# Kernel tuning notes

Hardware: AMD Instinct MI355X
Metric: run time of the kernel (lower is better)

The kernel has to match this reference:

```python
import jax, jax.numpy as jnp
import numpy as np

I_DECAY = 0.95
STAG_THRESH = 0.95
MAX_GATE = 0.6
MIN_I_GATE = 0.25
EPS = 1e-12


def setup_inputs() -> dict:
    key = jax.random.key(0)
    ks = jax.random.split(key, 9)
    B, T, D_IN, D_OUT = 4, 2048, 2048, 2048
    x = jax.random.normal(ks[0], (B, T, D_IN), dtype=jnp.float32)
    s = 1.0 / np.sqrt(D_IN)
    Wp = jax.random.uniform(ks[1], (D_IN, D_OUT), jnp.float32, -s, s)
    Wi = jax.random.uniform(ks[2], (D_IN, D_OUT), jnp.float32, -s, s) * 0.3
    Wd = jax.random.uniform(ks[3], (D_IN, D_OUT), jnp.float32, -s, s) * 0.3
    gate_w = jax.random.uniform(ks[4], (D_IN, 3), jnp.float32, -s, s)
    gate_b = jnp.array([0.5, 0.0, 0.0], dtype=jnp.float32)
    kick_vec = jax.random.normal(ks[5], (D_OUT,), dtype=jnp.float32) * 0.01
    kick_w = jax.random.uniform(ks[6], (D_IN, 1), jnp.float32, -s, s)
    kick_b = jnp.full((1,), -2.0, dtype=jnp.float32)
    bias = jnp.zeros((D_OUT,), dtype=jnp.float32)
    return {"x": x, "Wp": Wp, "Wi": Wi, "Wd": Wd, "gate_w": gate_w,
            "gate_b": gate_b, "kick_vec": kick_vec, "kick_w": kick_w,
            "kick_b": kick_b, "bias": bias}


def _ema_integral(x, decay):
    # x: [B,T,D] -> time-major scan; integral[0] = x[0]
    xt = jnp.swapaxes(x, 0, 1)  # [T,B,D]

    def step(carry, xcur):
        new = decay * carry + (1.0 - decay) * xcur
        return new, new

    init = xt[0]
    _, rest = jax.lax.scan(step, init, xt[1:])
    integral = jnp.concatenate([init[None], rest], axis=0)
    return jnp.swapaxes(integral, 0, 1)  # [B,T,D]


def reference(x, Wp, Wi, Wd, gate_w, gate_b, kick_vec, kick_w, kick_b, bias):
    B, T, D = x.shape
    # --- EMA integral (linear recurrence over T) ---
    integral = _ema_integral(x, I_DECAY)

    # --- stagnation-aware derivative ---
    diff = jnp.concatenate(
        [jnp.zeros_like(x[:, :1]), x[:, 1:] - x[:, :-1]], axis=1)
    x_norm = x / jnp.maximum(
        jnp.linalg.norm(x, axis=-1, keepdims=True), EPS)
    cos_sim = jnp.concatenate(
        [jnp.zeros((B, 1), x.dtype),
         jnp.sum(x_norm[:, 1:] * x_norm[:, :-1], axis=-1)], axis=1)  # [B,T]
    stagnation = (cos_sim > STAG_THRESH).astype(x.dtype)
    kick_strength = jax.nn.sigmoid(
        jnp.einsum('btd,do->bto', x, kick_w) + kick_b)[..., 0]  # [B,T]
    derivative = diff + (stagnation * kick_strength)[..., None] * kick_vec

    # --- gates: softmax -> clamp max -> clamp I min -> renormalize ---
    g = jax.nn.softmax(jnp.einsum('btd,dg->btg', x, gate_w) + gate_b, axis=-1)
    g = jnp.minimum(g, MAX_GATE)
    g = g.at[..., 1].set(jnp.maximum(g[..., 1], MIN_I_GATE))
    g = g / jnp.sum(g, axis=-1, keepdims=True)

    out = (g[..., 0:1] * jnp.einsum('btd,do->bto', x, Wp)
           + g[..., 1:2] * jnp.einsum('btd,do->bto', integral, Wi)
           + g[..., 2:3] * jnp.einsum('btd,do->bto', derivative, Wd))
    return out + bias
```

## Files before the change

kernel.cpp:

```cpp
#include <hip/hip_runtime.h>

#define DH 2048
#define TT 2048
#define BB 4
#define MROWS 8192
#define KTOT 6144
#define NCH 128
#define LCH 16
#define POW95_L 0.44012667f

typedef __attribute__((ext_vector_type(8))) short bf16x8;
typedef __attribute__((ext_vector_type(4))) float f32x4;

__device__ __forceinline__ unsigned short f2bf(float f) {
  union { float f; unsigned int u; } v; v.f = f;
  unsigned int u = v.u;
  return (unsigned short)((u + 0x7FFFu + ((u >> 16) & 1u)) >> 16);
}

__device__ __forceinline__ void gld16(const unsigned short* g, unsigned short* l) {
  __builtin_amdgcn_global_load_lds((const __attribute__((address_space(1))) void*)g,
                                   (__attribute__((address_space(3))) void*)l, 16, 0, 0);
}

__global__ __launch_bounds__(256) void prep_w(const float* __restrict__ Wp,
                                              const float* __restrict__ Wi,
                                              const float* __restrict__ Wd,
                                              const float* __restrict__ kick_vec,
                                              unsigned short* __restrict__ Wt,
                                              float* __restrict__ kvWd) {
  __shared__ float tile[64][65];
  int bid = blockIdx.x;
  int mat = bid >> 10;
  int t2 = bid & 1023;
  int dt = (t2 >> 5) * 64;
  int ot = (t2 & 31) * 64;
  const float* W = (mat == 0) ? Wp : ((mat == 1) ? Wi : Wd);
  int kbase = mat * DH;
  int tid = threadIdx.x;
  int r = tid >> 4;
  int c4 = (tid & 15) * 4;
#pragma unroll
  for (int i = 0; i < 4; ++i) {
    int rr = r + i * 16;
    float4 v = *(const float4*)&W[(size_t)(dt + rr) * DH + ot + c4];
    tile[rr][c4 + 0] = v.x; tile[rr][c4 + 1] = v.y;
    tile[rr][c4 + 2] = v.z; tile[rr][c4 + 3] = v.w;
  }
  __syncthreads();
  int o = tid >> 3;
  int d8 = (tid & 7) * 8;
#pragma unroll
  for (int pass = 0; pass < 2; ++pass) {
    int oo = o + pass * 32;
    union { unsigned short u[8]; uint4 v; } pk;
#pragma unroll
    for (int i = 0; i < 8; ++i) pk.u[i] = f2bf(tile[d8 + i][oo]);
    *(uint4*)&Wt[(size_t)(ot + oo) * KTOT + kbase + dt + d8] = pk.v;
  }
  if (mat == 2 && tid < 64) {
    float s = 0.f;
#pragma unroll 8
    for (int dd = 0; dd < 64; ++dd) s += kick_vec[dt + dd] * tile[dd][tid];
    atomicAdd(&kvWd[ot + tid], s);
  }
}

__global__ __launch_bounds__(256) void rowstats_kernel(const float* __restrict__ x,
                                                       const float* __restrict__ gate_w,
                                                       const float* __restrict__ gate_b,
                                                       const float* __restrict__ kick_w,
                                                       const float* __restrict__ kick_b,
                                                       float* __restrict__ rs) {
  int r = blockIdx.x;
  int t = r & (TT - 1);
  const float* xr = x + (size_t)r * DH;
  const float* xq = xr - DH;
  const bool hp = (t != 0);
  int tid = threadIdx.x;
  float a0 = 0, a1 = 0, a2 = 0, ak = 0, axx = 0, apx = 0, app = 0;
#pragma unroll
  for (int it = 0; it < 2; ++it) {
    int d0 = (tid + it * 256) * 4;
    float4 xv = *(const float4*)(xr + d0);
    float4 pv = hp ? *(const float4*)(xq + d0) : make_float4(0.f, 0.f, 0.f, 0.f);
    float4 q0 = *(const float4*)(gate_w + (size_t)d0 * 3);
    float4 q1 = *(const float4*)(gate_w + (size_t)d0 * 3 + 4);
    float4 q2 = *(const float4*)(gate_w + (size_t)d0 * 3 + 8);
    float4 kw = *(const float4*)(kick_w + d0);
    float xa[4] = {xv.x, xv.y, xv.z, xv.w};
    float pa[4] = {pv.x, pv.y, pv.z, pv.w};
    a0 += xa[0] * q0.x + xa[1] * q0.w + xa[2] * q1.z + xa[3] * q2.y;
    a1 += xa[0] * q0.y + xa[1] * q1.x + xa[2] * q1.w + xa[3] * q2.z;
    a2 += xa[0] * q0.z + xa[1] * q1.y + xa[2] * q2.x + xa[3] * q2.w;
    ak += xa[0] * kw.x + xa[1] * kw.y + xa[2] * kw.z + xa[3] * kw.w;
#pragma unroll
    for (int j = 0; j < 4; ++j) {
      axx += xa[j] * xa[j];
      apx += xa[j] * pa[j];
      app += pa[j] * pa[j];
    }
  }
#pragma unroll
  for (int off = 32; off > 0; off >>= 1) {
    a0 += __shfl_xor(a0, off); a1 += __shfl_xor(a1, off);
    a2 += __shfl_xor(a2, off); ak += __shfl_xor(ak, off);
    axx += __shfl_xor(axx, off); apx += __shfl_xor(apx, off);
    app += __shfl_xor(app, off);
  }
  __shared__ float red[4][7];
  int wv = tid >> 6;
  if ((tid & 63) == 0) {
    red[wv][0] = a0; red[wv][1] = a1; red[wv][2] = a2; red[wv][3] = ak;
    red[wv][4] = axx; red[wv][5] = apx; red[wv][6] = app;
  }
  __syncthreads();
  if (tid == 0) {
    float v[7];
#pragma unroll
    for (int i = 0; i < 7; ++i) v[i] = red[0][i] + red[1][i] + red[2][i] + red[3][i];
    float l0 = v[0] + gate_b[0], l1 = v[1] + gate_b[1], l2 = v[2] + gate_b[2];
    float mx = fmaxf(l0, fmaxf(l1, l2));
    float e0 = expf(l0 - mx), e1 = expf(l1 - mx), e2 = expf(l2 - mx);
    float inv = 1.f / (e0 + e1 + e2);
    float G0 = fminf(e0 * inv, 0.6f);
    float G1 = fminf(e1 * inv, 0.6f);
    float G2 = fminf(e2 * inv, 0.6f);
    G1 = fmaxf(G1, 0.25f);
    float inv2 = 1.f / (G0 + G1 + G2);
    G0 *= inv2; G1 *= inv2; G2 *= inv2;
    float ks = 1.f / (1.f + expf(-(v[3] + kick_b[0])));
    float nn = fmaxf(sqrtf(v[4]), 1e-12f) * fmaxf(sqrtf(v[6]), 1e-12f);
    float cs = hp ? (v[5] / nn) : 0.f;
    float cc = (cs > 0.95f) ? (G2 * ks) : 0.f;
    *(float4*)(rs + (size_t)r * 4) = make_float4(G0, G1, G2, cc);
  }
}

__global__ __launch_bounds__(256) void ema_carry(const float* __restrict__ x,
                                                 float* __restrict__ cp) {
  int gid = blockIdx.x * 256 + threadIdx.x;
  int d = (gid & 511) * 4;
  int ch = (gid >> 9) & (NCH - 1);
  int b = gid >> 16;
  const float* xp = x + ((size_t)b * TT + (size_t)ch * LCH) * DH + d;
  float J0, J1, J2, J3;
  int tstart;
  if (ch == 0) {
    float4 v = *(const float4*)xp;
    J0 = v.x; J1 = v.y; J2 = v.z; J3 = v.w;
    tstart = 1;
  } else {
    J0 = J1 = J2 = J3 = 0.f;
    tstart = 0;
  }
#pragma unroll 4
  for (int t = tstart; t < LCH; ++t) {
    float4 v = *(const float4*)(xp + (size_t)t * DH);
    J0 = 0.95f * J0 + 0.05f * v.x;
    J1 = 0.95f * J1 + 0.05f * v.y;
    J2 = 0.95f * J2 + 0.05f * v.z;
    J3 = 0.95f * J3 + 0.05f * v.w;
  }
  *(float4*)&cp[((size_t)b * NCH + ch) * DH + d] = make_float4(J0, J1, J2, J3);
}

__global__ __launch_bounds__(256) void ema_prefix(float* __restrict__ cp) {
  int gid = blockIdx.x * 256 + threadIdx.x;
  int d = (gid & 511) * 4;
  int b = gid >> 9;
  float4 run = make_float4(0.f, 0.f, 0.f, 0.f);
  for (int ch = 0; ch < NCH; ++ch) {
    size_t idx = ((size_t)b * NCH + ch) * DH + d;
    float4 cv = *(const float4*)&cp[idx];
    *(float4*)&cp[idx] = run;
    run.x = cv.x + POW95_L * run.x;
    run.y = cv.y + POW95_L * run.y;
    run.z = cv.z + POW95_L * run.z;
    run.w = cv.w + POW95_L * run.w;
  }
}

__global__ __launch_bounds__(256) void build_a(const float* __restrict__ x,
                                               const float* __restrict__ rs,
                                               const float* __restrict__ P,
                                               unsigned short* __restrict__ A) {
  int tid = threadIdx.x;
  int d = tid * 8;
  int ch = blockIdx.x & (NCH - 1);
  int b = blockIdx.x >> 7;
  int t0 = ch * LCH;
  const float* xp = x + ((size_t)b * TT + t0) * DH + d;
  unsigned short* Ar = A + ((size_t)b * TT + t0) * KTOT + d;
  float Pv[8], J[8], xprev[8];
  const bool first_chunk = (ch == 0);
  if (first_chunk) {
#pragma unroll
    for (int i = 0; i < 8; ++i) { Pv[i] = 0.f; xprev[i] = 0.f; }
  } else {
    float4 p0 = *(const float4*)&P[((size_t)b * NCH + ch) * DH + d];
    float4 p1 = *(const float4*)&P[((size_t)b * NCH + ch) * DH + d + 4];
    Pv[0] = p0.x; Pv[1] = p0.y; Pv[2] = p0.z; Pv[3] = p0.w;
    Pv[4] = p1.x; Pv[5] = p1.y; Pv[6] = p1.z; Pv[7] = p1.w;
    float4 v0 = *(const float4*)(xp - DH);
    float4 v1 = *(const float4*)(xp - DH + 4);
    xprev[0] = v0.x; xprev[1] = v0.y; xprev[2] = v0.z; xprev[3] = v0.w;
    xprev[4] = v1.x; xprev[5] = v1.y; xprev[6] = v1.z; xprev[7] = v1.w;
  }
#pragma unroll
  for (int i = 0; i < 8; ++i) J[i] = 0.f;
  float f = 1.f;
  float4 c0 = *(const float4*)(xp);
  float4 c1 = *(const float4*)(xp + 4);
#pragma unroll
  for (int tau = 0; tau < LCH; ++tau) {
    float4 n0, n1;
    if (tau < LCH - 1) {
      n0 = *(const float4*)(xp + (size_t)(tau + 1) * DH);
      n1 = *(const float4*)(xp + (size_t)(tau + 1) * DH + 4);
    }
    float xv[8] = {c0.x, c0.y, c0.z, c0.w, c1.x, c1.y, c1.z, c1.w};
    int r = b * TT + t0 + tau;
    float4 g = *(const float4*)&rs[(size_t)r * 4];
    const bool vfirst = first_chunk && (tau == 0);
    f *= 0.95f;
    union { unsigned short u[8]; uint4 v; } op, oi, od;
#pragma unroll
    for (int i = 0; i < 8; ++i) {
      if (vfirst) J[i] = xv[i];
      else J[i] = 0.95f * J[i] + 0.05f * xv[i];
      float I = J[i] + f * Pv[i];
      float diff = vfirst ? 0.f : (xv[i] - xprev[i]);
      op.u[i] = f2bf(g.x * xv[i]);
      oi.u[i] = f2bf(g.y * I);
      od.u[i] = f2bf(g.z * diff);
      xprev[i] = xv[i];
    }
    unsigned short* row = Ar + (size_t)tau * KTOT;
    *(uint4*)(row)          = op.v;
    *(uint4*)(row + DH)     = oi.v;
    *(uint4*)(row + 2 * DH) = od.v;
    c0 = n0; c1 = n1;
  }
}

__global__ __launch_bounds__(256) void gemm_kernel(const unsigned short* __restrict__ A,
                                                   const unsigned short* __restrict__ Bt,
                                                   const float* __restrict__ rs,
                                                   const float* __restrict__ kvWd,
                                                   const float* __restrict__ bias,
                                                   float* __restrict__ out) {
  __shared__ __align__(16) unsigned short lA[128 * 64];
  __shared__ __align__(16) unsigned short lB[128 * 64];
  const int tid = threadIdx.x;
  const int wave = tid >> 6, lane = tid & 63;
  const int bid = blockIdx.x;
  const int xcd = bid & 7;
  const int loc = bid >> 3;
  const int mblk = xcd * 8 + (loc & 7);
  const int nblk = loc >> 3;
  const int m0 = mblk * 128, n0 = nblk * 128;

  const int srow = wave * 32 + (lane >> 3);
  const int scol = ((lane & 7) ^ (lane >> 3)) * 8;
  const unsigned short* ga = A + (size_t)(m0 + srow) * KTOT + scol;
  const unsigned short* gb = Bt + (size_t)(n0 + srow) * KTOT + scol;
  unsigned short* la = &lA[(wave * 32) * 64];
  unsigned short* lb = &lB[(wave * 32) * 64];

  f32x4 acc[4][4] = {};
  const int arow = ((wave >> 1) * 64 + (lane & 15)) * 64;
  const int brow = ((wave & 1) * 64 + (lane & 15)) * 64;
  const int cbq = lane >> 4;
  const int swz = lane & 7;

  for (int k0 = 0; k0 < KTOT; k0 += 64) {
#pragma unroll
    for (int j = 0; j < 4; ++j) {
      gld16(ga + k0 + (size_t)j * 8 * KTOT, la + j * 8 * 64);
      gld16(gb + k0 + (size_t)j * 8 * KTOT, lb + j * 8 * 64);
    }
    __syncthreads();
#pragma unroll
    for (int kb = 0; kb < 2; ++kb) {
      const int kphys = ((kb * 4 + cbq) ^ swz) * 8;
      bf16x8 av[4], bv[4];
#pragma unroll
      for (int mi = 0; mi < 4; ++mi)
        av[mi] = *(const bf16x8*)&lA[arow + mi * 16 * 64 + kphys];
#pragma unroll
      for (int ni = 0; ni < 4; ++ni)
        bv[ni] = *(const bf16x8*)&lB[brow + ni * 16 * 64 + kphys];
#pragma unroll
      for (int mi = 0; mi < 4; ++mi)
#pragma unroll
        for (int ni = 0; ni < 4; ++ni)
          acc[mi][ni] = __builtin_amdgcn_mfma_f32_16x16x32_bf16(av[mi], bv[ni], acc[mi][ni], 0, 0, 0);
    }
    __syncthreads();
  }

  const int lr = lane >> 4, lc = lane & 15;
  const int mbase = m0 + (wave >> 1) * 64, nbase = n0 + (wave & 1) * 64;
  float cc[4][4];
#pragma unroll
  for (int mi = 0; mi < 4; ++mi)
#pragma unroll
    for (int rg = 0; rg < 4; ++rg)
      cc[mi][rg] = rs[(size_t)(mbase + mi * 16 + lr * 4 + rg) * 4 + 3];
#pragma unroll
  for (int ni = 0; ni < 4; ++ni) {
    const int n = nbase + ni * 16 + lc;
    const float kv = kvWd[n], bz = bias[n];
#pragma unroll
    for (int mi = 0; mi < 4; ++mi) {
#pragma unroll
      for (int rg = 0; rg < 4; ++rg) {
        const int m = mbase + mi * 16 + lr * 4 + rg;
        out[(size_t)m * DH + n] = acc[mi][ni][rg] + cc[mi][rg] * kv + bz;
      }
    }
  }
}

extern "C" void kernel_launch(void* const* d_in, const int* in_sizes, int n_in,
                              void* d_out, int out_size, void* d_ws, size_t ws_size,
                              hipStream_t stream) {
  const float* x        = (const float*)d_in[0];
  const float* Wp       = (const float*)d_in[1];
  const float* Wi       = (const float*)d_in[2];
  const float* Wd       = (const float*)d_in[3];
  const float* gate_w   = (const float*)d_in[4];
  const float* gate_b   = (const float*)d_in[5];
  const float* kick_vec = (const float*)d_in[6];
  const float* kick_w   = (const float*)d_in[7];
  const float* kick_b   = (const float*)d_in[8];
  const float* bias     = (const float*)d_in[9];
  float* out = (float*)d_out;

  char* ws = (char*)d_ws;
  unsigned short* Wt   = (unsigned short*)(ws + 0);
  unsigned short* Abuf = (unsigned short*)(ws + 25165824);
  float* rs    = (float*)(ws + 125829120);
  float* kvWd  = (float*)(ws + 125960192);
  float* cp    = (float*)(ws + 125968384);
  (void)ws_size; (void)in_sizes; (void)n_in; (void)out_size;

  hipMemsetAsync(kvWd, 0, DH * sizeof(float), stream);
  prep_w<<<dim3(3072), dim3(256), 0, stream>>>(Wp, Wi, Wd, kick_vec, Wt, kvWd);
  rowstats_kernel<<<dim3(8192), dim3(256), 0, stream>>>(x, gate_w, gate_b, kick_w, kick_b, rs);
  ema_carry<<<dim3(1024), dim3(256), 0, stream>>>(x, cp);
  ema_prefix<<<dim3(8), dim3(256), 0, stream>>>(cp);
  build_a<<<dim3(512), dim3(256), 0, stream>>>(x, rs, cp, Abuf);
  gemm_kernel<<<dim3(1024), dim3(256), 0, stream>>>(Abuf, Wt, rs, kvWd, bias, out);
}
```

Baseline: 438.8 us.

## Apply EMA and difference after the GEMM, exploiting linearity of the weight projections

Instead of building a K=6144 activation matrix of [g0·x, g1·integral, g2·diff] and multiplying it by stacked weights, the GEMM now computes x @ [Wp|Wi|Wd] with K=2048 into a bf16 intermediate Z. The EMA scan and the time difference are then applied to the Wi and Wd output columns, and gating, kick and bias are added in a final combine kernel. The EMA uses a two-level chunked prefix in the new zi_carry, zi_p1 and zi_p2 kernels. The wide activation build pass and the separate x-side EMA passes go away. In exchange there is a 6144-wide bf16 intermediate, written with scattered 2-byte stores in the GEMM epilogue, and extra rounding because the EMA runs on bf16 projected values and bf16 carries.

```diff
diff --git a/kernel.cpp b/kernel.cpp
--- a/kernel.cpp
+++ b/kernel.cpp
@@ -4,10 +4,11 @@
 #define TT 2048
 #define BB 4
 #define MROWS 8192
-#define KTOT 6144
+#define NZ 6144
 #define NCH 128
 #define LCH 16
-#define POW95_L 0.44012667f
+#define LAM 0.44012667f
+#define LAM2 1.982646e-06f
 
 typedef __attribute__((ext_vector_type(8))) short bf16x8;
 typedef __attribute__((ext_vector_type(4))) float f32x4;
@@ -17,7 +18,10 @@
   unsigned int u = v.u;
   return (unsigned short)((u + 0x7FFFu + ((u >> 16) & 1u)) >> 16);
 }
-
+__device__ __forceinline__ float bf2f(unsigned short u) {
+  union { unsigned int i; float f; } v; v.i = ((unsigned int)u) << 16;
+  return v.f;
+}
 __device__ __forceinline__ void gld16(const unsigned short* g, unsigned short* l) {
   __builtin_amdgcn_global_load_lds((const __attribute__((address_space(1))) void*)g,
                                    (__attribute__((address_space(3))) void*)l, 16, 0, 0);
@@ -36,7 +40,7 @@
   int dt = (t2 >> 5) * 64;
   int ot = (t2 & 31) * 64;
   const float* W = (mat == 0) ? Wp : ((mat == 1) ? Wi : Wd);
-  int kbase = mat * DH;
+  int nbase = mat * DH;
   int tid = threadIdx.x;
   int r = tid >> 4;
   int c4 = (tid & 15) * 4;
@@ -56,7 +60,7 @@
     union { unsigned short u[8]; uint4 v; } pk;
 #pragma unroll
     for (int i = 0; i < 8; ++i) pk.u[i] = f2bf(tile[d8 + i][oo]);
-    *(uint4*)&Wt[(size_t)(ot + oo) * KTOT + kbase + dt + d8] = pk.v;
+    *(uint4*)&Wt[(size_t)(nbase + ot + oo) * DH + dt + d8] = pk.v;
   }
   if (mat == 2 && tid < 64) {
     float s = 0.f;
@@ -66,12 +70,13 @@
   }
 }
 
-__global__ __launch_bounds__(256) void rowstats_kernel(const float* __restrict__ x,
-                                                       const float* __restrict__ gate_w,
-                                                       const float* __restrict__ gate_b,
-                                                       const float* __restrict__ kick_w,
-                                                       const float* __restrict__ kick_b,
-                                                       float* __restrict__ rs) {
+__global__ __launch_bounds__(256) void conv_x(const float* __restrict__ x,
+                                              const float* __restrict__ gate_w,
+                                              const float* __restrict__ gate_b,
+                                              const float* __restrict__ kick_w,
+                                              const float* __restrict__ kick_b,
+                                              float* __restrict__ rs,
+                                              unsigned short* __restrict__ A) {
   int r = blockIdx.x;
   int t = r & (TT - 1);
   const float* xr = x + (size_t)r * DH;
@@ -94,12 +99,15 @@
     a1 += xa[0] * q0.y + xa[1] * q1.x + xa[2] * q1.w + xa[3] * q2.z;
     a2 += xa[0] * q0.z + xa[1] * q1.y + xa[2] * q2.x + xa[3] * q2.w;
     ak += xa[0] * kw.x + xa[1] * kw.y + xa[2] * kw.z + xa[3] * kw.w;
+    union { unsigned short u[4]; uint2 v; } pk;
 #pragma unroll
     for (int j = 0; j < 4; ++j) {
       axx += xa[j] * xa[j];
       apx += xa[j] * pa[j];
       app += pa[j] * pa[j];
-    }
+      pk.u[j] = f2bf(xa[j]);
+    }
+    *(uint2*)&A[(size_t)r * DH + d0] = pk.v;
   }
 #pragma unroll
   for (int off = 32; off > 0; off >>= 1) {
@@ -137,119 +145,9 @@
   }
 }
 
-__global__ __launch_bounds__(256) void ema_carry(const float* __restrict__ x,
-                                                 float* __restrict__ cp) {
-  int gid = blockIdx.x * 256 + threadIdx.x;
-  int d = (gid & 511) * 4;
-  int ch = (gid >> 9) & (NCH - 1);
-  int b = gid >> 16;
-  const float* xp = x + ((size_t)b * TT + (size_t)ch * LCH) * DH + d;
-  float J0, J1, J2, J3;
-  int tstart;
-  if (ch == 0) {
-    float4 v = *(const float4*)xp;
-    J0 = v.x; J1 = v.y; J2 = v.z; J3 = v.w;
-    tstart = 1;
-  } else {
-    J0 = J1 = J2 = J3 = 0.f;
-    tstart = 0;
-  }
-#pragma unroll 4
-  for (int t = tstart; t < LCH; ++t) {
-    float4 v = *(const float4*)(xp + (size_t)t * DH);
-    J0 = 0.95f * J0 + 0.05f * v.x;
-    J1 = 0.95f * J1 + 0.05f * v.y;
-    J2 = 0.95f * J2 + 0.05f * v.z;
-    J3 = 0.95f * J3 + 0.05f * v.w;
-  }
-  *(float4*)&cp[((size_t)b * NCH + ch) * DH + d] = make_float4(J0, J1, J2, J3);
-}
-
-__global__ __launch_bounds__(256) void ema_prefix(float* __restrict__ cp) {
-  int gid = blockIdx.x * 256 + threadIdx.x;
-  int d = (gid & 511) * 4;
-  int b = gid >> 9;
-  float4 run = make_float4(0.f, 0.f, 0.f, 0.f);
-  for (int ch = 0; ch < NCH; ++ch) {
-    size_t idx = ((size_t)b * NCH + ch) * DH + d;
-    float4 cv = *(const float4*)&cp[idx];
-    *(float4*)&cp[idx] = run;
-    run.x = cv.x + POW95_L * run.x;
-    run.y = cv.y + POW95_L * run.y;
-    run.z = cv.z + POW95_L * run.z;
-    run.w = cv.w + POW95_L * run.w;
-  }
-}
-
-__global__ __launch_bounds__(256) void build_a(const float* __restrict__ x,
-                                               const float* __restrict__ rs,
-                                               const float* __restrict__ P,
-                                               unsigned short* __restrict__ A) {
-  int tid = threadIdx.x;
-  int d = tid * 8;
-  int ch = blockIdx.x & (NCH - 1);
-  int b = blockIdx.x >> 7;
-  int t0 = ch * LCH;
-  const float* xp = x + ((size_t)b * TT + t0) * DH + d;
-  unsigned short* Ar = A + ((size_t)b * TT + t0) * KTOT + d;
-  float Pv[8], J[8], xprev[8];
-  const bool first_chunk = (ch == 0);
-  if (first_chunk) {
-#pragma unroll
-    for (int i = 0; i < 8; ++i) { Pv[i] = 0.f; xprev[i] = 0.f; }
-  } else {
-    float4 p0 = *(const float4*)&P[((size_t)b * NCH + ch) * DH + d];
-    float4 p1 = *(const float4*)&P[((size_t)b * NCH + ch) * DH + d + 4];
-    Pv[0] = p0.x; Pv[1] = p0.y; Pv[2] = p0.z; Pv[3] = p0.w;
-    Pv[4] = p1.x; Pv[5] = p1.y; Pv[6] = p1.z; Pv[7] = p1.w;
-    float4 v0 = *(const float4*)(xp - DH);
-    float4 v1 = *(const float4*)(xp - DH + 4);
-    xprev[0] = v0.x; xprev[1] = v0.y; xprev[2] = v0.z; xprev[3] = v0.w;
-    xprev[4] = v1.x; xprev[5] = v1.y; xprev[6] = v1.z; xprev[7] = v1.w;
-  }
-#pragma unroll
-  for (int i = 0; i < 8; ++i) J[i] = 0.f;
-  float f = 1.f;
-  float4 c0 = *(const float4*)(xp);
-  float4 c1 = *(const float4*)(xp + 4);
-#pragma unroll
-  for (int tau = 0; tau < LCH; ++tau) {
-    float4 n0, n1;
-    if (tau < LCH - 1) {
-      n0 = *(const float4*)(xp + (size_t)(tau + 1) * DH);
-      n1 = *(const float4*)(xp + (size_t)(tau + 1) * DH + 4);
-    }
-    float xv[8] = {c0.x, c0.y, c0.z, c0.w, c1.x, c1.y, c1.z, c1.w};
-    int r = b * TT + t0 + tau;
-    float4 g = *(const float4*)&rs[(size_t)r * 4];
-    const bool vfirst = first_chunk && (tau == 0);
-    f *= 0.95f;
-    union { unsigned short u[8]; uint4 v; } op, oi, od;
-#pragma unroll
-    for (int i = 0; i < 8; ++i) {
-      if (vfirst) J[i] = xv[i];
-      else J[i] = 0.95f * J[i] + 0.05f * xv[i];
-      float I = J[i] + f * Pv[i];
-      float diff = vfirst ? 0.f : (xv[i] - xprev[i]);
-      op.u[i] = f2bf(g.x * xv[i]);
-      oi.u[i] = f2bf(g.y * I);
-      od.u[i] = f2bf(g.z * diff);
-      xprev[i] = xv[i];
-    }
-    unsigned short* row = Ar + (size_t)tau * KTOT;
-    *(uint4*)(row)          = op.v;
-    *(uint4*)(row + DH)     = oi.v;
-    *(uint4*)(row + 2 * DH) = od.v;
-    c0 = n0; c1 = n1;
-  }
-}
-
 __global__ __launch_bounds__(256) void gemm_kernel(const unsigned short* __restrict__ A,
                                                    const unsigned short* __restrict__ Bt,
-                                                   const float* __restrict__ rs,
-                                                   const float* __restrict__ kvWd,
-                                                   const float* __restrict__ bias,
-                                                   float* __restrict__ out) {
+                                                   unsigned short* __restrict__ Z) {
   __shared__ __align__(16) unsigned short lA[128 * 64];
   __shared__ __align__(16) unsigned short lB[128 * 64];
   const int tid = threadIdx.x;
@@ -263,8 +161,8 @@
 
   const int srow = wave * 32 + (lane >> 3);
   const int scol = ((lane & 7) ^ (lane >> 3)) * 8;
-  const unsigned short* ga = A + (size_t)(m0 + srow) * KTOT + scol;
-  const unsigned short* gb = Bt + (size_t)(n0 + srow) * KTOT + scol;
+  const unsigned short* ga = A + (size_t)(m0 + srow) * DH + scol;
+  const unsigned short* gb = Bt + (size_t)(n0 + srow) * DH + scol;
   unsigned short* la = &lA[(wave * 32) * 64];
   unsigned short* lb = &lB[(wave * 32) * 64];
 
@@ -274,11 +172,11 @@
   const int cbq = lane >> 4;
   const int swz = lane & 7;
 
-  for (int k0 = 0; k0 < KTOT; k0 += 64) {
+  for (int k0 = 0; k0 < DH; k0 += 64) {
 #pragma unroll
     for (int j = 0; j < 4; ++j) {
-      gld16(ga + k0 + (size_t)j * 8 * KTOT, la + j * 8 * 64);
-      gld16(gb + k0 + (size_t)j * 8 * KTOT, lb + j * 8 * 64);
+      gld16(ga + k0 + (size_t)j * 8 * DH, la + j * 8 * 64);
+      gld16(gb + k0 + (size_t)j * 8 * DH, lb + j * 8 * 64);
     }
     __syncthreads();
 #pragma unroll
@@ -302,24 +200,172 @@
 
   const int lr = lane >> 4, lc = lane & 15;
   const int mbase = m0 + (wave >> 1) * 64, nbase = n0 + (wave & 1) * 64;
-  float cc[4][4];
-#pragma unroll
-  for (int mi = 0; mi < 4; ++mi)
-#pragma unroll
-    for (int rg = 0; rg < 4; ++rg)
-      cc[mi][rg] = rs[(size_t)(mbase + mi * 16 + lr * 4 + rg) * 4 + 3];
 #pragma unroll
   for (int ni = 0; ni < 4; ++ni) {
     const int n = nbase + ni * 16 + lc;
-    const float kv = kvWd[n], bz = bias[n];
 #pragma unroll
     for (int mi = 0; mi < 4; ++mi) {
 #pragma unroll
       for (int rg = 0; rg < 4; ++rg) {
         const int m = mbase + mi * 16 + lr * 4 + rg;
-        out[(size_t)m * DH + n] = acc[mi][ni][rg] + cc[mi][rg] * kv + bz;
+        Z[(size_t)m * NZ + n] = f2bf(acc[mi][ni][rg]);
       }
     }
+  }
+}
+
+__global__ __launch_bounds__(256) void zi_carry(const unsigned short* __restrict__ Z,
+                                                unsigned short* __restrict__ cpb) {
+  int gid = blockIdx.x * 256 + threadIdx.x;
+  int n = (gid & 511) * 4;
+  int ch = (gid >> 9) & (NCH - 1);
+  int b = gid >> 16;
+  const unsigned short* zp = Z + ((size_t)(b * TT + ch * LCH)) * NZ + DH + n;
+  float J0, J1, J2, J3;
+  int tstart;
+  if (ch == 0) {
+    union { unsigned short u[4]; uint2 v; } c;
+    c.v = *(const uint2*)zp;
+    J0 = bf2f(c.u[0]); J1 = bf2f(c.u[1]); J2 = bf2f(c.u[2]); J3 = bf2f(c.u[3]);
+    tstart = 1;
+  } else {
+    J0 = J1 = J2 = J3 = 0.f;
+    tstart = 0;
+  }
+#pragma unroll 4
+  for (int t = tstart; t < LCH; ++t) {
+    union { unsigned short u[4]; uint2 v; } c;
+    c.v = *(const uint2*)(zp + (size_t)t * NZ);
+    J0 = 0.95f * J0 + 0.05f * bf2f(c.u[0]);
+    J1 = 0.95f * J1 + 0.05f * bf2f(c.u[1]);
+    J2 = 0.95f * J2 + 0.05f * bf2f(c.u[2]);
+    J3 = 0.95f * J3 + 0.05f * bf2f(c.u[3]);
+  }
+  union { unsigned short u[4]; uint2 v; } o;
+  o.u[0] = f2bf(J0); o.u[1] = f2bf(J1); o.u[2] = f2bf(J2); o.u[3] = f2bf(J3);
+  *(uint2*)&cpb[((size_t)b * NCH + ch) * DH + n] = o.v;
+}
+
+__global__ __launch_bounds__(256) void zi_p1(unsigned short* __restrict__ cpb,
+                                             float* __restrict__ gc) {
+  int gid = blockIdx.x * 256 + threadIdx.x;
+  int n = (gid & 511) * 4;
+  int g = (gid >> 9) & 7;
+  int b = gid >> 12;
+  float r0 = 0, r1 = 0, r2 = 0, r3 = 0;
+#pragma unroll
+  for (int j = 0; j < 16; ++j) {
+    size_t idx = ((size_t)b * NCH + g * 16 + j) * DH + n;
+    union { unsigned short u[4]; uint2 v; } c;
+    c.v = *(const uint2*)&cpb[idx];
+    float c0 = bf2f(c.u[0]), c1 = bf2f(c.u[1]), c2 = bf2f(c.u[2]), c3 = bf2f(c.u[3]);
+    union { unsigned short u[4]; uint2 v; } o;
+    o.u[0] = f2bf(r0); o.u[1] = f2bf(r1); o.u[2] = f2bf(r2); o.u[3] = f2bf(r3);
+    *(uint2*)&cpb[idx] = o.v;
+    r0 = c0 + LAM * r0; r1 = c1 + LAM * r1;
+    r2 = c2 + LAM * r2; r3 = c3 + LAM * r3;
+  }
+  *(float4*)&gc[((size_t)b * 8 + g) * DH + n] = make_float4(r0, r1, r2, r3);
+}
+
+__global__ __launch_bounds__(256) void zi_p2(float* __restrict__ gc) {
+  int gid = blockIdx.x * 256 + threadIdx.x;
+  int n = (gid & 511) * 4;
+  int b = gid >> 9;
+  float4 run = make_float4(0.f, 0.f, 0.f, 0.f);
+#pragma unroll
+  for (int g = 0; g < 8; ++g) {
+    size_t idx = ((size_t)b * 8 + g) * DH + n;
+    float4 old = *(const float4*)&gc[idx];
+    *(float4*)&gc[idx] = run;
+    run.x = old.x + LAM2 * run.x;
+    run.y = old.y + LAM2 * run.y;
+    run.z = old.z + LAM2 * run.z;
+    run.w = old.w + LAM2 * run.w;
+  }
+}
+
+__global__ __launch_bounds__(256) void final_combine(const unsigned short* __restrict__ Z,
+                                                     const float* __restrict__ rs,
+                                                     const unsigned short* __restrict__ cpb,
+                                                     const float* __restrict__ gc,
+                                                     const float* __restrict__ kvWd,
+                                                     const float* __restrict__ bias,
+                                                     float* __restrict__ out) {
+  int tid = threadIdx.x;
+  int n = tid * 8;
+  int ch = blockIdx.x & (NCH - 1);
+  int b = blockIdx.x >> 7;
+  int r0 = b * TT + ch * LCH;
+  const unsigned short* zb = Z + (size_t)r0 * NZ + n;
+  const bool first_chunk = (ch == 0);
+
+  int g = ch >> 4, j = ch & 15;
+  float pw = 1.f;
+  for (int i = 0; i < j; ++i) pw *= LAM;
+  float Pv[8];
+  {
+    union { unsigned short u[8]; uint4 v; } c;
+    c.v = *(const uint4*)&cpb[((size_t)b * NCH + ch) * DH + n];
+    float4 gp0 = *(const float4*)&gc[((size_t)b * 8 + g) * DH + n];
+    float4 gp1 = *(const float4*)&gc[((size_t)b * 8 + g) * DH + n + 4];
+    float gp[8] = {gp0.x, gp0.y, gp0.z, gp0.w, gp1.x, gp1.y, gp1.z, gp1.w};
+#pragma unroll
+    for (int i = 0; i < 8; ++i) Pv[i] = bf2f(c.u[i]) + pw * gp[i];
+  }
+  float kv[8], bz[8];
+  {
+    float4 k0 = *(const float4*)&kvWd[n], k1 = *(const float4*)&kvWd[n + 4];
+    float4 b0 = *(const float4*)&bias[n], b1 = *(const float4*)&bias[n + 4];
+    kv[0]=k0.x; kv[1]=k0.y; kv[2]=k0.z; kv[3]=k0.w; kv[4]=k1.x; kv[5]=k1.y; kv[6]=k1.z; kv[7]=k1.w;
+    bz[0]=b0.x; bz[1]=b0.y; bz[2]=b0.z; bz[3]=b0.w; bz[4]=b1.x; bz[5]=b1.y; bz[6]=b1.z; bz[7]=b1.w;
+  }
+  float zdp[8];
+  if (!first_chunk) {
+    union { unsigned short u[8]; uint4 v; } c;
+    c.v = *(const uint4*)(zb - NZ + 2 * DH);
+#pragma unroll
+    for (int i = 0; i < 8; ++i) zdp[i] = bf2f(c.u[i]);
+  } else {
+#pragma unroll
+    for (int i = 0; i < 8; ++i) zdp[i] = 0.f;
+  }
+  float J[8];
+#pragma unroll
+  for (int i = 0; i < 8; ++i) J[i] = 0.f;
+  float f = 1.f;
+  uint4 cp = *(const uint4*)(zb);
+  uint4 ci = *(const uint4*)(zb + DH);
+  uint4 cd = *(const uint4*)(zb + 2 * DH);
+#pragma unroll
+  for (int tau = 0; tau < LCH; ++tau) {
+    uint4 np, ni, nd;
+    if (tau < LCH - 1) {
+      const unsigned short* zn = zb + (size_t)(tau + 1) * NZ;
+      np = *(const uint4*)(zn);
+      ni = *(const uint4*)(zn + DH);
+      nd = *(const uint4*)(zn + 2 * DH);
+    }
+    float4 gg = *(const float4*)&rs[(size_t)(r0 + tau) * 4];
+    union { unsigned short u[8]; uint4 v; } up, ui, ud;
+    up.v = cp; ui.v = ci; ud.v = cd;
+    const bool vfirst = first_chunk && (tau == 0);
+    f *= 0.95f;
+    float o[8];
+#pragma unroll
+    for (int i = 0; i < 8; ++i) {
+      float xp = bf2f(up.u[i]), xi = bf2f(ui.u[i]), xd = bf2f(ud.u[i]);
+      if (vfirst) J[i] = xi;
+      else J[i] = 0.95f * J[i] + 0.05f * xi;
+      float I = J[i] + f * Pv[i];
+      float diff = vfirst ? 0.f : (xd - zdp[i]);
+      o[i] = gg.x * xp + gg.y * I + gg.z * diff + gg.w * kv[i] + bz[i];
+      zdp[i] = xd;
+    }
+    float* orow = out + (size_t)(r0 + tau) * DH + n;
+    *(float4*)(orow) = make_float4(o[0], o[1], o[2], o[3]);
+    *(float4*)(orow + 4) = make_float4(o[4], o[5], o[6], o[7]);
+    cp = np; ci = ni; cd = nd;
   }
 }
 
@@ -339,18 +385,21 @@
   float* out = (float*)d_out;
 
   char* ws = (char*)d_ws;
-  unsigned short* Wt   = (unsigned short*)(ws + 0);
-  unsigned short* Abuf = (unsigned short*)(ws + 25165824);
-  float* rs    = (float*)(ws + 125829120);
-  float* kvWd  = (float*)(ws + 125960192);
-  float* cp    = (float*)(ws + 125968384);
+  unsigned short* Wt  = (unsigned short*)(ws + 0);
+  unsigned short* Z   = (unsigned short*)(ws + 25165824);
+  float* rs   = (float*)(ws + 125829120);
+  float* kvWd = (float*)(ws + 125960192);
+  unsigned short* cpb = (unsigned short*)(ws + 125968384);
+  float* gc   = (float*)(ws + 128065536);
+  unsigned short* A = (unsigned short*)d_out;
   (void)ws_size; (void)in_sizes; (void)n_in; (void)out_size;
 
   hipMemsetAsync(kvWd, 0, DH * sizeof(float), stream);
   prep_w<<<dim3(3072), dim3(256), 0, stream>>>(Wp, Wi, Wd, kick_vec, Wt, kvWd);
-  rowstats_kernel<<<dim3(8192), dim3(256), 0, stream>>>(x, gate_w, gate_b, kick_w, kick_b, rs);
-  ema_carry<<<dim3(1024), dim3(256), 0, stream>>>(x, cp);
-  ema_prefix<<<dim3(8), dim3(256), 0, stream>>>(cp);
-  build_a<<<dim3(512), dim3(256), 0, stream>>>(x, rs, cp, Abuf);
-  gemm_kernel<<<dim3(1024), dim3(256), 0, stream>>>(Abuf, Wt, rs, kvWd, bias, out);
-}
+  conv_x<<<dim3(8192), dim3(256), 0, stream>>>(x, gate_w, gate_b, kick_w, kick_b, rs, A);
+  gemm_kernel<<<dim3(3072), dim3(256), 0, stream>>>(A, Wt, Z);
+  zi_carry<<<dim3(1024), dim3(256), 0, stream>>>(Z, cpb);
+  zi_p1<<<dim3(64), dim3(256), 0, stream>>>(cpb, gc);
+  zi_p2<<<dim3(8), dim3(256), 0, stream>>>(gc);
+  final_combine<<<dim3(512), dim3(256), 0, stream>>>(Z, rs, cpb, gc, kvWd, bias, out);
+}
```

New measurement: 430.6 us. About the same (-1.9%).
